# Performance work log

Hardware: AMD Instinct MI355X
Metric: run time of the kernel (lower is better)

Reference implementation:

```python
import jax, jax.numpy as jnp
import numpy as np

B, L, T = 512, 512, 128
START, STOP = T - 2, T - 1   # tag_dict: '<START>'->126, '<STOP>'->127
NEG = -10000.0


def setup_inputs() -> dict:
    key = jax.random.key(0)
    k1, k2, k3, k4 = jax.random.split(key, 4)
    feats = jax.random.normal(k1, (B, L, T), dtype=jnp.float32)
    # learned transition matrix, initialized as in CRF.__init__
    trans = jax.random.normal(k2, (T, T), dtype=jnp.float32)
    trans = trans.at[START, :].set(NEG).at[:, STOP].set(NEG)
    tags = jax.random.randint(k3, (B, L), 0, T - 2)          # gold tags, no START/STOP
    lens = jax.random.randint(k4, (B,), 1, L + 1)            # actual lengths in [1, L]
    return {"feats": feats, "transitions": trans, "tags": tags, "lens": lens}


def _crf_loss(feats, transitions, tags, lens):
    Bn, Ln, Tn = feats.shape

    # ---- forward algorithm (log partition) ----
    init = jnp.full((Tn,), NEG, dtype=feats.dtype).at[START].set(0.0)
    fv0 = jnp.broadcast_to(init, (Bn, Tn))

    def step(fv, xs):
        emit, i = xs                                  # emit: [B, T]
        # tag_var[b, next, prev] = emit[b,next] + trans[next,prev] + fv[b,prev]
        tv = emit[:, :, None] + transitions[None, :, :] + fv[:, None, :]
        new = jax.scipy.special.logsumexp(tv, axis=2)  # [B, T]
        # freeze fv once past each sentence's length (== gathering at index lens)
        fv = jnp.where((i < lens)[:, None], new, fv)
        return fv, None

    fv, _ = jax.lax.scan(step, fv0, (jnp.swapaxes(feats, 0, 1), jnp.arange(Ln)))
    terminal = fv + transitions[START][None, :]       # matches original (uses START row)
    forward_score = jax.scipy.special.logsumexp(terminal, axis=1)  # [B]

    # ---- gold sentence score ----
    start_col = jnp.full((Bn, 1), START, dtype=tags.dtype)
    stop_col = jnp.full((Bn, 1), STOP, dtype=tags.dtype)
    pad_start = jnp.concatenate([start_col, tags], axis=1)   # [B, L+1]
    pad_stop = jnp.concatenate([tags, stop_col], axis=1)     # [B, L+1]
    pos = jnp.arange(Ln + 1)[None, :]
    pad_stop = jnp.where(pos >= lens[:, None], STOP, pad_stop)

    trans_terms = transitions[pad_stop, pad_start]           # [B, L+1]
    trans_sum = jnp.sum(jnp.where(pos <= lens[:, None], trans_terms, 0.0), axis=1)
    emit_terms = jnp.take_along_axis(feats, tags[:, :, None], axis=2)[..., 0]  # [B, L]
    emit_mask = jnp.arange(Ln)[None, :] < lens[:, None]
    emit_sum = jnp.sum(jnp.where(emit_mask, emit_terms, 0.0), axis=1)
    gold_score = trans_sum + emit_sum

    return jnp.mean(forward_score - gold_score)


def reference(feats, transitions, tags, lens):
    return _crf_loss(feats, transitions, tags, lens)
```

## Files before the change

kernel.cpp:

```cpp
#include <hip/hip_runtime.h>

#define Bsz 512
#define Lsz 512
#define Tsz 128
#define TAG_START 126
#define TAG_STOP 127
#define SPB 16
#define UPITCH 136

typedef __attribute__((ext_vector_type(8))) short short8;
typedef __attribute__((ext_vector_type(4))) float f32x4;

__device__ __forceinline__ void lds_barrier() {
  asm volatile("s_waitcnt lgkmcnt(0)\n\ts_barrier" ::: "memory");
}
__device__ __forceinline__ unsigned pack_bf16(float lo, float hi) {
  unsigned a = (__float_as_uint(lo) + 0x8000u) >> 16;
  unsigned b = (__float_as_uint(hi) + 0x8000u) & 0xFFFF0000u;
  return b | a;
}
__device__ __forceinline__ float bf16lo(unsigned d) { return __uint_as_float(d << 16); }
__device__ __forceinline__ float bf16hi(unsigned d) { return __uint_as_float(d & 0xFFFF0000u); }

__global__ __launch_bounds__(512) void crf_fwd_kernel(
    const float* __restrict__ feats, const float* __restrict__ trans,
    const int* __restrict__ tags, const int* __restrict__ lens,
    float* __restrict__ diff_out)
{
  __shared__ __align__(16) unsigned short u_lds[2][SPB][UPITCH];
  __shared__ float fv_sh[Tsz][SPB];
  __shared__ float red[4][SPB];
  __shared__ float gold_sh[SPB];
  __shared__ int msh;

  const int g    = blockIdx.x;
  const int tid  = threadIdx.x;
  const int w    = tid >> 6;
  const int lane = tid & 63;
  const int q    = lane >> 4;
  const int s    = lane & 15;
  const int seq  = g * SPB + s;
  const int lenc = lens[seq];
  const int lim  = lenc - 1;

  if (tid == 0) msh = 1;
  __syncthreads();
  if (tid < SPB) atomicMax(&msh, lens[g * SPB + tid]);
  for (int i = tid; i < 2 * SPB * UPITCH; i += 512)
    ((unsigned short*)u_lds)[i] = 0;
  __syncthreads();
  const int maxlen = msh;
  if (tid < SPB) u_lds[0][tid][TAG_START] = 0x3F80;
  __syncthreads();

  short8 af[4];
  {
    const float* tr = trans + (size_t)(w * 16 + s) * Tsz + q * 8;
    #pragma unroll
    for (int c = 0; c < 4; ++c) {
      float4 x = *(const float4*)(tr + c * 32);
      float4 y = *(const float4*)(tr + c * 32 + 4);
      union { unsigned u[4]; short8 v; } cv;
      cv.u[0] = pack_bf16(__expf(x.x), __expf(x.y));
      cv.u[1] = pack_bf16(__expf(x.z), __expf(x.w));
      cv.u[2] = pack_bf16(__expf(y.x), __expf(y.y));
      cv.u[3] = pack_bf16(__expf(y.z), __expf(y.w));
      af[c] = cv.v;
    }
  }

  const float* fp = feats + (size_t)seq * (Lsz * Tsz) + w * 16 + 4 * q;

  float4 pa0, pa1, pa2, pa3;
  { int r1 = (1 < lim) ? 1 : lim, r2 = (2 < lim) ? 2 : lim, r3 = (3 < lim) ? 3 : lim;
    if (lim < 1) r1 = r2 = r3 = lim;
    pa0 = *(const float4*)(fp);
    pa1 = *(const float4*)(fp + ((size_t)r1 << 7));
    pa2 = *(const float4*)(fp + ((size_t)r2 << 7));
    pa3 = *(const float4*)(fp + ((size_t)r3 << 7)); }

  float ee[4] = {__expf(pa0.x), __expf(pa0.y), __expf(pa0.z), __expf(pa0.w)};

  float m_run = 0.0f, mcap = 0.0f;
  float ucap[4];
  #pragma unroll
  for (int i = 0; i < 4; ++i) ucap[i] = 1.0f;

#define STEP(T, PA, NA, BR, BW)                                                \
  { const int t_ = (T);                                                        \
    short8 bq0 = *(const short8*)&u_lds[BR][s][0 * 32 + q * 8];                \
    short8 bq1 = *(const short8*)&u_lds[BR][s][1 * 32 + q * 8];                \
    short8 bq2 = *(const short8*)&u_lds[BR][s][2 * 32 + q * 8];                \
    short8 bq3 = *(const short8*)&u_lds[BR][s][3 * 32 + q * 8];                \
    unsigned ud = *(const unsigned*)&u_lds[BR][s][0];                          \
    int tp = t_ + 4; tp = (tp < lim) ? tp : lim;                               \
    PA = *(const float4*)(fp + ((size_t)tp << 7));                             \
    f32x4 acc = {0.f, 0.f, 0.f, 0.f};                                          \
    acc = __builtin_amdgcn_mfma_f32_16x16x32_bf16(af[0], bq0, acc, 0,0,0);     \
    acc = __builtin_amdgcn_mfma_f32_16x16x32_bf16(af[1], bq1, acc, 0,0,0);     \
    acc = __builtin_amdgcn_mfma_f32_16x16x32_bf16(af[2], bq2, acc, 0,0,0);     \
    acc = __builtin_amdgcn_mfma_f32_16x16x32_bf16(af[3], bq3, acc, 0,0,0);     \
    float eta = bf16lo(ud) + bf16hi(ud);                                       \
    if (t_ == 0) eta = 1.0f;                                                   \
    float rce = __builtin_amdgcn_rcpf(eta);                                    \
    bool capt = (t_ == lim);                                                   \
    float uv[4];                                                               \
    _Pragma("unroll") for (int i = 0; i < 4; ++i)                              \
      uv[i] = acc[i] * rce * ee[i];                                            \
    _Pragma("unroll") for (int i = 0; i < 4; ++i)                              \
      ucap[i] = capt ? uv[i] : ucap[i];                                        \
    m_run += __logf(eta);                                                      \
    mcap = capt ? m_run : mcap;                                                \
    unsigned short* dst = &u_lds[BW][s][0];                                    \
    uint2 pk; pk.x = pack_bf16(uv[0], uv[1]); pk.y = pack_bf16(uv[2], uv[3]);  \
    *(uint2*)&dst[w * 16 + 4 * q] = pk;                                        \
    ee[0] = __expf(NA.x); ee[1] = __expf(NA.y);                                \
    ee[2] = __expf(NA.z); ee[3] = __expf(NA.w);                                \
    lds_barrier();                                                             \
  }

  for (int t = 0; t < maxlen; t += 4) {
    STEP(t + 0, pa0, pa1, 0, 1)
    STEP(t + 1, pa1, pa2, 1, 0)
    STEP(t + 2, pa2, pa3, 0, 1)
    STEP(t + 3, pa3, pa0, 1, 0)
  }
#undef STEP

  __syncthreads();

  #pragma unroll
  for (int r = 0; r < 4; ++r) {
    int row = w * 16 + 4 * q + r;
    fv_sh[row][s] = __logf(ucap[r]) + mcap + trans[TAG_START * Tsz + row];
  }
  __syncthreads();

  float fwd_score = 0.f;
  float fvv[8];
  if (w < 4) {
    #pragma unroll
    for (int i = 0; i < 2; ++i)
      #pragma unroll
      for (int r = 0; r < 4; ++r)
        fvv[i * 4 + r] = fv_sh[(2 * w + i) * 16 + 4 * q + r][s];
    float mx = fvv[0];
    #pragma unroll
    for (int i = 1; i < 8; ++i) mx = fmaxf(mx, fvv[i]);
    mx = fmaxf(mx, __shfl_xor(mx, 16, 64));
    mx = fmaxf(mx, __shfl_xor(mx, 32, 64));
    if (q == 0) red[w][s] = mx;
  }
  __syncthreads();
  float gmx = 0.f;
  if (w < 4) gmx = fmaxf(fmaxf(red[0][s], red[1][s]), fmaxf(red[2][s], red[3][s]));
  __syncthreads();
  if (w < 4) {
    float se = 0.f;
    #pragma unroll
    for (int i = 0; i < 8; ++i) se += __expf(fvv[i] - gmx);
    se += __shfl_xor(se, 16, 64);
    se += __shfl_xor(se, 32, 64);
    if (q == 0) red[w][s] = se;
  }
  __syncthreads();
  if (w < 4)
    fwd_score = gmx + __logf((red[0][s] + red[1][s]) + (red[2][s] + red[3][s]));

  if (w < 4) {
    int jj = 4 * w + q;
    int gs2 = g * SPB + jj;
    int lenj = lens[gs2];
    const int* tg = tags + (size_t)gs2 * Lsz;
    const float* fbj = feats + (size_t)gs2 * (Lsz * Tsz);
    float acc = 0.f;
    for (int pos = s; pos <= lenj; pos += 16) {
      int st = (pos == 0)    ? TAG_START : tg[pos - 1];
      int et = (pos == lenj) ? TAG_STOP  : tg[pos];
      acc += trans[et * Tsz + st];
    }
    for (int l = s; l < lenj; l += 16)
      acc += fbj[(size_t)l * Tsz + tg[l]];
    #pragma unroll
    for (int off = 1; off < 16; off <<= 1) acc += __shfl_xor(acc, off, 64);
    if (s == 0) gold_sh[jj] = acc;
  }
  __syncthreads();
  if (w == 0 && q == 0)
    diff_out[g * SPB + s] = fwd_score - gold_sh[s];
}

__global__ __launch_bounds__(Bsz) void crf_final_kernel(
    const float* __restrict__ diff, float* __restrict__ out)
{
  int tid = threadIdx.x;
  float v = diff[tid];
  __shared__ float wred[8];
  float sum = v;
  #pragma unroll
  for (int off = 32; off > 0; off >>= 1) sum += __shfl_down(sum, off, 64);
  int wave = tid >> 6, lane = tid & 63;
  if (lane == 0) wred[wave] = sum;
  __syncthreads();
  if (tid == 0) {
    float t = 0.f;
    #pragma unroll
    for (int i = 0; i < 8; ++i) t += wred[i];
    out[0] = t * (1.0f / Bsz);
  }
}

extern "C" void kernel_launch(void* const* d_in, const int* in_sizes, int n_in,
                              void* d_out, int out_size, void* d_ws, size_t ws_size,
                              hipStream_t stream) {
  const float* feats = (const float*)d_in[0];
  const float* trans = (const float*)d_in[1];
  const int*   tags  = (const int*)d_in[2];
  const int*   lens  = (const int*)d_in[3];
  float* out  = (float*)d_out;
  float* diff = (float*)d_ws;

  crf_fwd_kernel<<<Bsz / SPB, 512, 0, stream>>>(feats, trans, tags, lens, diff);
  crf_final_kernel<<<1, Bsz, 0, stream>>>(diff, out);
}
```

Baseline: 399.5 us.

## Warp-specialize CRF forward: one compute wave, three producer waves prefetching exp(feats)

The recurrence moves onto a single wave that holds all eight 16-row transition tiles in registers and runs the 32 MFMAs per step itself. Three producer waves load feats, exponentiate them and write them into a shared-memory ring in blocks of six timesteps. This replaces the per-step workgroup barrier of the old eight-wave split with one barrier per six steps. In exchange, each step's MFMA chain is serialized on one wave and register pressure rises sharply (af[8][4], ucap[8][4]). Producers also exponentiate every timestep up to maxlen for all 16 sequences.

```diff
diff --git a/kernel.cpp b/kernel.cpp
--- a/kernel.cpp
+++ b/kernel.cpp
@@ -7,13 +7,13 @@
 #define TAG_STOP 127
 #define SPB 16
 #define UPITCH 136
+#define EPITCH 132
+#define NSLOT 12
+#define SBLK 6
 
 typedef __attribute__((ext_vector_type(8))) short short8;
 typedef __attribute__((ext_vector_type(4))) float f32x4;
 
-__device__ __forceinline__ void lds_barrier() {
-  asm volatile("s_waitcnt lgkmcnt(0)\n\ts_barrier" ::: "memory");
-}
 __device__ __forceinline__ unsigned pack_bf16(float lo, float hi) {
   unsigned a = (__float_as_uint(lo) + 0x8000u) >> 16;
   unsigned b = (__float_as_uint(hi) + 0x8000u) & 0xFFFF0000u;
@@ -22,14 +22,13 @@
 __device__ __forceinline__ float bf16lo(unsigned d) { return __uint_as_float(d << 16); }
 __device__ __forceinline__ float bf16hi(unsigned d) { return __uint_as_float(d & 0xFFFF0000u); }
 
-__global__ __launch_bounds__(512) void crf_fwd_kernel(
+__global__ __launch_bounds__(256, 1) void crf_fwd_kernel(
     const float* __restrict__ feats, const float* __restrict__ trans,
     const int* __restrict__ tags, const int* __restrict__ lens,
     float* __restrict__ diff_out)
 {
   __shared__ __align__(16) unsigned short u_lds[2][SPB][UPITCH];
-  __shared__ float fv_sh[Tsz][SPB];
-  __shared__ float red[4][SPB];
+  __shared__ __align__(16) float ee_ring[NSLOT][SPB][EPITCH];
   __shared__ float gold_sh[SPB];
   __shared__ int msh;
 
@@ -40,150 +39,182 @@
   const int q    = lane >> 4;
   const int s    = lane & 15;
   const int seq  = g * SPB + s;
-  const int lenc = lens[seq];
-  const int lim  = lenc - 1;
+  const int lim  = lens[seq] - 1;
 
   if (tid == 0) msh = 1;
   __syncthreads();
   if (tid < SPB) atomicMax(&msh, lens[g * SPB + tid]);
-  for (int i = tid; i < 2 * SPB * UPITCH; i += 512)
+  for (int i = tid; i < 2 * SPB * UPITCH; i += 256)
     ((unsigned short*)u_lds)[i] = 0;
   __syncthreads();
   const int maxlen = msh;
   if (tid < SPB) u_lds[0][tid][TAG_START] = 0x3F80;
-  __syncthreads();
-
-  short8 af[4];
+
+  const int nblk = (maxlen + SBLK - 1) / SBLK;
+
+  auto produce = [&](int t, int slot) {
+    int tc = t < Lsz ? t : (Lsz - 1);
+    int seq16 = lane >> 2, rb = (lane & 3) * 32;
+    const float* src = feats + ((size_t)(g * SPB + seq16) * Lsz + tc) * Tsz + rb;
+    float* dst = &ee_ring[slot][seq16][rb];
+    #pragma unroll
+    for (int k2 = 0; k2 < 8; ++k2) {
+      float4 v = *(const float4*)(src + 4 * k2);
+      float4 e;
+      e.x = __expf(v.x); e.y = __expf(v.y); e.z = __expf(v.z); e.w = __expf(v.w);
+      *(float4*)(dst + 4 * k2) = e;
+    }
+  };
+
+  short8 af[8][4];
+  float ucap[8][4];
+  float m_run = 0.f, mcap = 0.f;
+
+  if (w == 0) {
+    #pragma unroll
+    for (int i = 0; i < 8; ++i) {
+      const float* tr = trans + (size_t)(i * 16 + s) * Tsz + q * 8;
+      #pragma unroll
+      for (int c = 0; c < 4; ++c) {
+        float4 x = *(const float4*)(tr + c * 32);
+        float4 y = *(const float4*)(tr + c * 32 + 4);
+        union { unsigned u[4]; short8 v; } cv;
+        cv.u[0] = pack_bf16(__expf(x.x), __expf(x.y));
+        cv.u[1] = pack_bf16(__expf(x.z), __expf(x.w));
+        cv.u[2] = pack_bf16(__expf(y.x), __expf(y.y));
+        cv.u[3] = pack_bf16(__expf(y.z), __expf(y.w));
+        af[i][c] = cv.v;
+      }
+      ucap[i][0] = ucap[i][1] = ucap[i][2] = ucap[i][3] = 1.0f;
+    }
+  } else {
+    for (int t = w - 1; t < SBLK; t += 3) produce(t, t);
+  }
+  __syncthreads();
+
+  for (int blk = 0; blk < nblk; ++blk) {
+    const int sb = (blk & 1) ? SBLK : 0;
+    if (w == 0) {
+      #pragma unroll
+      for (int k = 0; k < SBLK; ++k) {
+        const int t = blk * SBLK + k;
+        const int rbuf = k & 1;
+        float4 ev[8];
+        const float* er = &ee_ring[sb + k][s][4 * q];
+        #pragma unroll
+        for (int i = 0; i < 8; ++i) ev[i] = *(const float4*)(er + 16 * i);
+        const unsigned short* ub = &u_lds[rbuf][s][0];
+        short8 bq0 = *(const short8*)(ub + 0 * 32 + q * 8);
+        short8 bq1 = *(const short8*)(ub + 1 * 32 + q * 8);
+        short8 bq2 = *(const short8*)(ub + 2 * 32 + q * 8);
+        short8 bq3 = *(const short8*)(ub + 3 * 32 + q * 8);
+        unsigned ud = *(const unsigned*)ub;
+        f32x4 acc[8];
+        #pragma unroll
+        for (int i = 0; i < 8; ++i) {
+          f32x4 a = {0.f, 0.f, 0.f, 0.f};
+          a = __builtin_amdgcn_mfma_f32_16x16x32_bf16(af[i][0], bq0, a, 0, 0, 0);
+          a = __builtin_amdgcn_mfma_f32_16x16x32_bf16(af[i][1], bq1, a, 0, 0, 0);
+          a = __builtin_amdgcn_mfma_f32_16x16x32_bf16(af[i][2], bq2, a, 0, 0, 0);
+          a = __builtin_amdgcn_mfma_f32_16x16x32_bf16(af[i][3], bq3, a, 0, 0, 0);
+          acc[i] = a;
+        }
+        float eta = bf16lo(ud) + bf16hi(ud);
+        if (t == 0) eta = 1.0f;
+        float rce = __builtin_amdgcn_rcpf(eta);
+        float uv[8][4];
+        #pragma unroll
+        for (int i = 0; i < 8; ++i) {
+          uv[i][0] = acc[i][0] * rce * ev[i].x;
+          uv[i][1] = acc[i][1] * rce * ev[i].y;
+          uv[i][2] = acc[i][2] * rce * ev[i].z;
+          uv[i][3] = acc[i][3] * rce * ev[i].w;
+        }
+        m_run += __logf(eta);
+        if (t == lim) {
+          #pragma unroll
+          for (int i = 0; i < 8; ++i) {
+            ucap[i][0] = uv[i][0]; ucap[i][1] = uv[i][1];
+            ucap[i][2] = uv[i][2]; ucap[i][3] = uv[i][3];
+          }
+          mcap = m_run;
+        }
+        unsigned short* dstp = &u_lds[rbuf ^ 1][s][0];
+        #pragma unroll
+        for (int i = 0; i < 8; ++i) {
+          uint2 pk;
+          pk.x = pack_bf16(uv[i][0], uv[i][1]);
+          pk.y = pack_bf16(uv[i][2], uv[i][3]);
+          *(uint2*)(dstp + 16 * i + 4 * q) = pk;
+        }
+      }
+    } else {
+      const int b2 = (blk + 1) * SBLK;
+      const int sb2 = ((blk + 1) & 1) ? SBLK : 0;
+      for (int j = w - 1; j < SBLK; j += 3) produce(b2 + j, sb2 + j);
+    }
+    __syncthreads();
+  }
+
+  float fwd_score = 0.f;
+  if (w == 0) {
+    float fvv[8][4];
+    const float* tr2 = trans + TAG_START * Tsz + 4 * q;
+    #pragma unroll
+    for (int i = 0; i < 8; ++i) {
+      float4 tv = *(const float4*)(tr2 + 16 * i);
+      fvv[i][0] = __logf(ucap[i][0]) + mcap + tv.x;
+      fvv[i][1] = __logf(ucap[i][1]) + mcap + tv.y;
+      fvv[i][2] = __logf(ucap[i][2]) + mcap + tv.z;
+      fvv[i][3] = __logf(ucap[i][3]) + mcap + tv.w;
+    }
+    float redm[4], reds[4];
+    #pragma unroll
+    for (int w2 = 0; w2 < 4; ++w2) {
+      float mx = fvv[2 * w2][0];
+      mx = fmaxf(mx, fvv[2 * w2][1]);
+      mx = fmaxf(mx, fvv[2 * w2][2]);
+      mx = fmaxf(mx, fvv[2 * w2][3]);
+      mx = fmaxf(mx, fvv[2 * w2 + 1][0]);
+      mx = fmaxf(mx, fvv[2 * w2 + 1][1]);
+      mx = fmaxf(mx, fvv[2 * w2 + 1][2]);
+      mx = fmaxf(mx, fvv[2 * w2 + 1][3]);
+      mx = fmaxf(mx, __shfl_xor(mx, 16, 64));
+      mx = fmaxf(mx, __shfl_xor(mx, 32, 64));
+      redm[w2] = mx;
+    }
+    float gmx = fmaxf(fmaxf(redm[0], redm[1]), fmaxf(redm[2], redm[3]));
+    #pragma unroll
+    for (int w2 = 0; w2 < 4; ++w2) {
+      float se = 0.f;
+      #pragma unroll
+      for (int r = 0; r < 4; ++r) se += __expf(fvv[2 * w2][r] - gmx);
+      #pragma unroll
+      for (int r = 0; r < 4; ++r) se += __expf(fvv[2 * w2 + 1][r] - gmx);
+      se += __shfl_xor(se, 16, 64);
+      se += __shfl_xor(se, 32, 64);
+      reds[w2] = se;
+    }
+    fwd_score = gmx + __logf((reds[0] + reds[1]) + (reds[2] + reds[3]));
+  }
+
   {
-    const float* tr = trans + (size_t)(w * 16 + s) * Tsz + q * 8;
-    #pragma unroll
-    for (int c = 0; c < 4; ++c) {
-      float4 x = *(const float4*)(tr + c * 32);
-      float4 y = *(const float4*)(tr + c * 32 + 4);
-      union { unsigned u[4]; short8 v; } cv;
-      cv.u[0] = pack_bf16(__expf(x.x), __expf(x.y));
-      cv.u[1] = pack_bf16(__expf(x.z), __expf(x.w));
-      cv.u[2] = pack_bf16(__expf(y.x), __expf(y.y));
-      cv.u[3] = pack_bf16(__expf(y.z), __expf(y.w));
-      af[c] = cv.v;
-    }
-  }
-
-  const float* fp = feats + (size_t)seq * (Lsz * Tsz) + w * 16 + 4 * q;
-
-  float4 pa0, pa1, pa2, pa3;
-  { int r1 = (1 < lim) ? 1 : lim, r2 = (2 < lim) ? 2 : lim, r3 = (3 < lim) ? 3 : lim;
-    if (lim < 1) r1 = r2 = r3 = lim;
-    pa0 = *(const float4*)(fp);
-    pa1 = *(const float4*)(fp + ((size_t)r1 << 7));
-    pa2 = *(const float4*)(fp + ((size_t)r2 << 7));
-    pa3 = *(const float4*)(fp + ((size_t)r3 << 7)); }
-
-  float ee[4] = {__expf(pa0.x), __expf(pa0.y), __expf(pa0.z), __expf(pa0.w)};
-
-  float m_run = 0.0f, mcap = 0.0f;
-  float ucap[4];
-  #pragma unroll
-  for (int i = 0; i < 4; ++i) ucap[i] = 1.0f;
-
-#define STEP(T, PA, NA, BR, BW)                                                \
-  { const int t_ = (T);                                                        \
-    short8 bq0 = *(const short8*)&u_lds[BR][s][0 * 32 + q * 8];                \
-    short8 bq1 = *(const short8*)&u_lds[BR][s][1 * 32 + q * 8];                \
-    short8 bq2 = *(const short8*)&u_lds[BR][s][2 * 32 + q * 8];                \
-    short8 bq3 = *(const short8*)&u_lds[BR][s][3 * 32 + q * 8];                \
-    unsigned ud = *(const unsigned*)&u_lds[BR][s][0];                          \
-    int tp = t_ + 4; tp = (tp < lim) ? tp : lim;                               \
-    PA = *(const float4*)(fp + ((size_t)tp << 7));                             \
-    f32x4 acc = {0.f, 0.f, 0.f, 0.f};                                          \
-    acc = __builtin_amdgcn_mfma_f32_16x16x32_bf16(af[0], bq0, acc, 0,0,0);     \
-    acc = __builtin_amdgcn_mfma_f32_16x16x32_bf16(af[1], bq1, acc, 0,0,0);     \
-    acc = __builtin_amdgcn_mfma_f32_16x16x32_bf16(af[2], bq2, acc, 0,0,0);     \
-    acc = __builtin_amdgcn_mfma_f32_16x16x32_bf16(af[3], bq3, acc, 0,0,0);     \
-    float eta = bf16lo(ud) + bf16hi(ud);                                       \
-    if (t_ == 0) eta = 1.0f;                                                   \
-    float rce = __builtin_amdgcn_rcpf(eta);                                    \
-    bool capt = (t_ == lim);                                                   \
-    float uv[4];                                                               \
-    _Pragma("unroll") for (int i = 0; i < 4; ++i)                              \
-      uv[i] = acc[i] * rce * ee[i];                                            \
-    _Pragma("unroll") for (int i = 0; i < 4; ++i)                              \
-      ucap[i] = capt ? uv[i] : ucap[i];                                        \
-    m_run += __logf(eta);                                                      \
-    mcap = capt ? m_run : mcap;                                                \
-    unsigned short* dst = &u_lds[BW][s][0];                                    \
-    uint2 pk; pk.x = pack_bf16(uv[0], uv[1]); pk.y = pack_bf16(uv[2], uv[3]);  \
-    *(uint2*)&dst[w * 16 + 4 * q] = pk;                                        \
-    ee[0] = __expf(NA.x); ee[1] = __expf(NA.y);                                \
-    ee[2] = __expf(NA.z); ee[3] = __expf(NA.w);                                \
-    lds_barrier();                                                             \
-  }
-
-  for (int t = 0; t < maxlen; t += 4) {
-    STEP(t + 0, pa0, pa1, 0, 1)
-    STEP(t + 1, pa1, pa2, 1, 0)
-    STEP(t + 2, pa2, pa3, 0, 1)
-    STEP(t + 3, pa3, pa0, 1, 0)
-  }
-#undef STEP
-
-  __syncthreads();
-
-  #pragma unroll
-  for (int r = 0; r < 4; ++r) {
-    int row = w * 16 + 4 * q + r;
-    fv_sh[row][s] = __logf(ucap[r]) + mcap + trans[TAG_START * Tsz + row];
-  }
-  __syncthreads();
-
-  float fwd_score = 0.f;
-  float fvv[8];
-  if (w < 4) {
-    #pragma unroll
-    for (int i = 0; i < 2; ++i)
-      #pragma unroll
-      for (int r = 0; r < 4; ++r)
-        fvv[i * 4 + r] = fv_sh[(2 * w + i) * 16 + 4 * q + r][s];
-    float mx = fvv[0];
-    #pragma unroll
-    for (int i = 1; i < 8; ++i) mx = fmaxf(mx, fvv[i]);
-    mx = fmaxf(mx, __shfl_xor(mx, 16, 64));
-    mx = fmaxf(mx, __shfl_xor(mx, 32, 64));
-    if (q == 0) red[w][s] = mx;
-  }
-  __syncthreads();
-  float gmx = 0.f;
-  if (w < 4) gmx = fmaxf(fmaxf(red[0][s], red[1][s]), fmaxf(red[2][s], red[3][s]));
-  __syncthreads();
-  if (w < 4) {
-    float se = 0.f;
-    #pragma unroll
-    for (int i = 0; i < 8; ++i) se += __expf(fvv[i] - gmx);
-    se += __shfl_xor(se, 16, 64);
-    se += __shfl_xor(se, 32, 64);
-    if (q == 0) red[w][s] = se;
-  }
-  __syncthreads();
-  if (w < 4)
-    fwd_score = gmx + __logf((red[0][s] + red[1][s]) + (red[2][s] + red[3][s]));
-
-  if (w < 4) {
     int jj = 4 * w + q;
     int gs2 = g * SPB + jj;
     int lenj = lens[gs2];
     const int* tg = tags + (size_t)gs2 * Lsz;
     const float* fbj = feats + (size_t)gs2 * (Lsz * Tsz);
-    float acc = 0.f;
+    float gacc = 0.f;
     for (int pos = s; pos <= lenj; pos += 16) {
       int st = (pos == 0)    ? TAG_START : tg[pos - 1];
       int et = (pos == lenj) ? TAG_STOP  : tg[pos];
-      acc += trans[et * Tsz + st];
+      gacc += trans[et * Tsz + st];
     }
     for (int l = s; l < lenj; l += 16)
-      acc += fbj[(size_t)l * Tsz + tg[l]];
-    #pragma unroll
-    for (int off = 1; off < 16; off <<= 1) acc += __shfl_xor(acc, off, 64);
-    if (s == 0) gold_sh[jj] = acc;
+      gacc += fbj[(size_t)l * Tsz + tg[l]];
+    #pragma unroll
+    for (int off = 1; off < 16; off <<= 1) gacc += __shfl_xor(gacc, off, 64);
+    if (s == 0) gold_sh[jj] = gacc;
   }
   __syncthreads();
   if (w == 0 && q == 0)
@@ -220,6 +251,6 @@
   float* out  = (float*)d_out;
   float* diff = (float*)d_ws;
 
-  crf_fwd_kernel<<<Bsz / SPB, 512, 0, stream>>>(feats, trans, tags, lens, diff);
+  crf_fwd_kernel<<<Bsz / SPB, 256, 0, stream>>>(feats, trans, tags, lens, diff);
   crf_final_kernel<<<1, Bsz, 0, stream>>>(diff, out);
 }
```

After: 553.2 us. 38.5% more time.
